# Kernel tuning notes

Measured on AMD Instinct MI355X. Metric: run time of the kernel, lower is better.

The kernel has to match this reference:

```python
import jax, jax.numpy as jnp
import numpy as np

B, NPER, F, D, E, NUM_STEPS = 256, 512, 256, 32, 524288, 4
N = B * NPER
INIT_TAU, TAU_SCALE, STEP_ALPHA = 0.1, 0.5, 5.0


def setup_inputs() -> dict:
    key = jax.random.key(0)
    ks = jax.random.split(key, 10)
    x_start = jax.random.uniform(ks[0], (N,), jnp.float32, 0.1, 1.0)   # strictly positive iterate
    x_solution = jax.random.uniform(ks[1], (N,), jnp.float32, 0.0, 1.0)
    q = jax.random.normal(ks[2], (N,), jnp.float32)
    edge_src = jax.random.randint(ks[3], (E,), 0, N, jnp.int32)
    edge_dst = jax.random.randint(ks[4], (E,), 0, N, jnp.int32)
    vals_batch = jnp.repeat(jnp.arange(B, dtype=jnp.int32), NPER)      # equal-sized graphs
    proj_matrix = jax.random.normal(ks[5], (B, NPER, F), jnp.float32) / np.float32(np.sqrt(NPER))
    W_in = jax.random.normal(ks[6], (2, D), jnp.float32) / np.float32(np.sqrt(2.0))
    b_in = jnp.zeros((D,), jnp.float32)
    W_msg = jax.random.normal(ks[7], (D, D), jnp.float32) / np.float32(np.sqrt(D))
    b_msg = jnp.zeros((D,), jnp.float32)
    W_out = jax.random.normal(ks[8], (D, 1), jnp.float32) / np.float32(np.sqrt(D))
    b_out = jnp.zeros((1,), jnp.float32)
    return {"x_start": x_start, "x_solution": x_solution, "q": q,
            "proj_matrix": proj_matrix, "W_in": W_in, "b_in": b_in,
            "W_msg": W_msg, "b_msg": b_msg, "W_out": W_out, "b_out": b_out,
            "edge_src": edge_src, "edge_dst": edge_dst, "vals_batch": vals_batch}


def _l1_normalize(x, batch):
    # per-graph L1 normalization: x / sum_i |x_i| over the graph segment
    s = jax.ops.segment_sum(jnp.abs(x), batch, num_segments=B)
    return x / (s[batch] + 1e-12)


def _line_search(x, d, batch, max_alpha):
    # largest per-graph alpha s.t. x + alpha*d >= 0, capped at max_alpha
    ratio = jnp.where(d < 0, x / jnp.maximum(-d, 1e-12), max_alpha)
    a = jnp.clip(jax.ops.segment_min(ratio, batch, num_segments=B), 0.0, max_alpha)
    return a[batch]  # gathered back to per-node


def _gnn(xs, q, edge_src, edge_dst, W_in, b_in, W_msg, b_msg, W_out, b_out):
    h = jax.nn.relu(jnp.stack([xs, q], axis=-1) @ W_in + b_in)      # [N, D]
    m = h[edge_src] @ W_msg + b_msg                                  # [E, D]
    agg = jax.ops.segment_sum(m, edge_dst, num_segments=N)          # [N, D]
    h2 = jax.nn.relu(h + agg)
    return h2 @ W_out[:, 0] + b_out[0]                               # [N]


def reference(x_start, x_solution, q, proj_matrix, W_in, b_in, W_msg, b_msg,
              W_out, b_out, edge_src, edge_dst, vals_batch):
    tau = INIT_TAU
    xs = x_start
    preds, labels = [], []
    for _ in range(NUM_STEPS):
        pred = _gnn(xs, q, edge_src, edge_dst, W_in, b_in, W_msg, b_msg, W_out, b_out)
        preds.append(pred)
        labels.append(_l1_normalize(x_solution - xs, vals_batch))
        p = _l1_normalize(jax.lax.stop_gradient(pred), vals_batch)   # .detach() in torch
        direction = p + 3.0 * tau / (xs + tau)
        tau = max(tau * TAU_SCALE, 1e-5)
        # to_dense_batch with equal graph sizes == reshape; project onto nullspace basis
        dd = direction.reshape(B, NPER)
        df = jnp.einsum('bnf,bn->bf', proj_matrix, dd)               # [B, F]
        pproj = jnp.einsum('bnf,bf->bn', proj_matrix, df).reshape(-1)  # [N]
        alpha = _line_search(xs, pproj, vals_batch, STEP_ALPHA) * 0.995
        xs = xs + alpha * pproj
    return jnp.stack(preds, axis=1), jnp.stack(labels, axis=1)       # each [N, NUM_STEPS]
```

## Files before the change

### kernel.cpp

```cpp
#include <hip/hip_runtime.h>

#define BB 256
#define NPER 512
#define FF 256
#define DD 32
#define EE 524288
#define NN (BB*NPER)
#define NSTEPS 4

__device__ __forceinline__ float bflo(unsigned u) { return __uint_as_float(u << 16); }
__device__ __forceinline__ float bfhi(unsigned u) { return __uint_as_float(u & 0xFFFF0000u); }
__device__ __forceinline__ unsigned rtn_bf16(unsigned u) {
    return (u + 0x7FFFu + ((u >> 16) & 1u)) >> 16;
}


__global__ void k_degpack(const int* __restrict__ dst, unsigned* __restrict__ deg,
                          const float* __restrict__ xs0, const float* __restrict__ q,
                          float2* __restrict__ xq) {
    int t = blockIdx.x * blockDim.x + threadIdx.x;
    if (t < NN) { float2 v; v.x = xs0[t]; v.y = q[t]; xq[t] = v; }
    atomicAdd(&deg[dst[t]], 1u);
}

__global__ void k_bsum(const unsigned* __restrict__ deg, unsigned* __restrict__ bsum) {
    __shared__ unsigned r[256];
    int t = threadIdx.x;
    r[t] = deg[blockIdx.x * 256 + t];
    __syncthreads();
    for (int o = 128; o > 0; o >>= 1) { if (t < o) r[t] += r[t + o]; __syncthreads(); }
    if (t == 0) bsum[blockIdx.x] = r[0];
}

__global__ void k_scanb(const unsigned* __restrict__ bsum, unsigned* __restrict__ bbase) {
    __shared__ unsigned r[512];
    int t = threadIdx.x;
    unsigned own = bsum[t];
    r[t] = own;
    __syncthreads();
    for (int o = 1; o < 512; o <<= 1) {
        unsigned v = (t >= o) ? r[t - o] : 0u;
        __syncthreads();
        r[t] += v;
        __syncthreads();
    }
    bbase[t] = r[t] - own;
}

__global__ void k_offsets(const unsigned* __restrict__ deg, const unsigned* __restrict__ bbase,
                          unsigned* __restrict__ rowstart, unsigned* __restrict__ cursor) {
    __shared__ unsigned r[256];
    int t = threadIdx.x;
    int i = blockIdx.x * 256 + t;
    unsigned d = deg[i];
    r[t] = d;
    __syncthreads();
    for (int o = 1; o < 256; o <<= 1) {
        unsigned v = (t >= o) ? r[t - o] : 0u;
        __syncthreads();
        r[t] += v;
        __syncthreads();
    }
    unsigned excl = r[t] - d + bbase[blockIdx.x];
    rowstart[i] = excl;
    cursor[i] = excl;
}

__global__ void k_fill(const int* __restrict__ src, const int* __restrict__ dst,
                       unsigned* __restrict__ cursor, int* __restrict__ csr_src) {
    int e = blockIdx.x * blockDim.x + threadIdx.x;
    unsigned pos = atomicAdd(&cursor[dst[e]], 1u);
    csr_src[pos] = src[e];
}

__global__ __launch_bounds__(256) void k_cast(const float* __restrict__ Pf,
                                              unsigned short* __restrict__ Pbf) {
    size_t idx = ((size_t)blockIdx.x * 256 + threadIdx.x) * 8;
    float4 a = *(const float4*)(Pf + idx);
    float4 c = *(const float4*)(Pf + idx + 4);
    uint4 o;
    o.x = rtn_bf16(__float_as_uint(a.x)) | (rtn_bf16(__float_as_uint(a.y)) << 16);
    o.y = rtn_bf16(__float_as_uint(a.z)) | (rtn_bf16(__float_as_uint(a.w)) << 16);
    o.z = rtn_bf16(__float_as_uint(c.x)) | (rtn_bf16(__float_as_uint(c.y)) << 16);
    o.w = rtn_bf16(__float_as_uint(c.z)) | (rtn_bf16(__float_as_uint(c.w)) << 16);
    *(uint4*)(Pbf + idx) = o;
}


__global__ void k_node_g(const float2* __restrict__ xq,
                         const float* __restrict__ Win, const float* __restrict__ bin,
                         const unsigned* __restrict__ rowstart, const unsigned* __restrict__ deg,
                         const int* __restrict__ csr_src,
                         const float* __restrict__ Wmsg, const float* __restrict__ bmsg,
                         const float* __restrict__ Wout, const float* __restrict__ bout,
                         float* __restrict__ pred, float* __restrict__ out_preds, int step) {
    int tid = threadIdx.x;
    int d = tid & 31;
    int i = blockIdx.x * 8 + (tid >> 5);
    float w0 = Win[d], w1 = Win[DD + d], b0 = bin[d];
    float wcol[DD];
    #pragma unroll
    for (int k = 0; k < DD; ++k) wcol[k] = Wmsg[k * DD + d];
    unsigned rs = rowstart[i];
    unsigned dg = deg[i];
    unsigned nfull = dg < 32u ? dg : 32u;
    float xv = 0.f, qv = 0.f;
    if ((unsigned)d < nfull) {
        int sv = csr_src[rs + d];
        float2 v = xq[sv];
        xv = v.x; qv = v.y;
    }
    float s = 0.f;
    for (unsigned j = 0; j < nfull; ++j) {
        float xj = __shfl(xv, (int)j, 32);
        float qj = __shfl(qv, (int)j, 32);
        s += fmaxf(xj * w0 + qj * w1 + b0, 0.f);
    }
    for (unsigned j = 32; j < dg; ++j) {
        int sv = csr_src[rs + j];
        float2 v = xq[sv];
        s += fmaxf(v.x * w0 + v.y * w1 + b0, 0.f);
    }
    float2 self = xq[i];
    float hval = fmaxf(self.x * w0 + self.y * w1 + b0, 0.f);
    float agg = (float)dg * bmsg[d];
    #pragma unroll
    for (int k = 0; k < DD; ++k) agg += __shfl(s, k, 32) * wcol[k];
    float h2 = fmaxf(hval + agg, 0.f);
    float v = h2 * Wout[d];
    for (int o = 16; o > 0; o >>= 1) v += __shfl_down(v, o, 32);
    if (d == 0) {
        float pr = v + bout[0];
        pred[i] = pr;
        out_preds[i * NSTEPS + step] = pr;
    }
}

__global__ __launch_bounds__(1024) void k_proj(const unsigned short* __restrict__ Pbf,
                                               float2* __restrict__ xq,
                                               const float* __restrict__ xsol,
                                               const float* __restrict__ pred,
                                               float* __restrict__ out_labels,
                                               float tau, int step) {
    __shared__ float dd_l[NPER], x_l[NPER], pp_l[NPER];
    __shared__ float sl[16 * FF];
    __shared__ float dfl[FF];
    __shared__ float redA[16], redB[16], wmin[16];
    int b = blockIdx.x;
    int t = threadIdx.x;
    int w = t >> 6, lane = t & 63;
    int gbase = b * NPER;

    float x = 0.f, r = 0.f, p = 0.f, a1 = 0.f, a2 = 0.f;
    if (t < NPER) {
        x = xq[gbase + t].x;
        r = xsol[gbase + t] - x;
        p = pred[gbase + t];
        a1 = fabsf(r); a2 = fabsf(p);
    }
    #pragma unroll
    for (int o = 32; o > 0; o >>= 1) {
        a1 += __shfl_down(a1, o, 64);
        a2 += __shfl_down(a2, o, 64);
    }
    if (lane == 0) { redA[w] = a1; redB[w] = a2; }
    __syncthreads();
    float Sr = 1e-12f, Sp = 1e-12f;
    #pragma unroll
    for (int k = 0; k < 16; ++k) { Sr += redA[k]; Sp += redB[k]; }
    if (t < NPER) {
        out_labels[(size_t)(gbase + t) * NSTEPS + step] = r / Sr;
        x_l[t] = x;
        dd_l[t] = p / Sp + 3.0f * tau / (x + tau);
    }
    __syncthreads();

    size_t pbase = ((size_t)(gbase + w * 32)) * FF + 4 * lane;
    const uint2* Pr = (const uint2*)(Pbf + pbase);
    unsigned pl[64];
    #pragma unroll
    for (int n = 0; n < 32; ++n) {
        uint2 pv = Pr[(size_t)n * 64];
        pl[2 * n] = pv.x; pl[2 * n + 1] = pv.y;
    }
    float4 acc = {0.f, 0.f, 0.f, 0.f};
    #pragma unroll
    for (int n = 0; n < 32; ++n) {
        float sc = dd_l[w * 32 + n];
        acc.x += bflo(pl[2 * n]) * sc;
        acc.y += bfhi(pl[2 * n]) * sc;
        acc.z += bflo(pl[2 * n + 1]) * sc;
        acc.w += bfhi(pl[2 * n + 1]) * sc;
    }
    ((float4*)sl)[w * 64 + lane] = acc;
    __syncthreads();
    if (t < FF) {
        float v = 0.f;
        #pragma unroll
        for (int k = 0; k < 16; ++k) v += sl[k * FF + t];
        dfl[t] = v;
    }
    __syncthreads();

    float4 dfv = ((const float4*)dfl)[lane];
    float mloc = 5.0f;
    #pragma unroll
    for (int n = 0; n < 32; ++n) {
        float pr = bflo(pl[2 * n]) * dfv.x + bfhi(pl[2 * n]) * dfv.y
                 + bflo(pl[2 * n + 1]) * dfv.z + bfhi(pl[2 * n + 1]) * dfv.w;
        #pragma unroll
        for (int o = 1; o < 64; o <<= 1) pr += __shfl_xor(pr, o, 64);
        if (lane == 0) pp_l[w * 32 + n] = pr;
        float xr = x_l[w * 32 + n];
        float ratio = (pr < 0.f) ? (xr / fmaxf(-pr, 1e-12f)) : 5.0f;
        mloc = fminf(mloc, ratio);
    }
    if (lane == 0) wmin[w] = mloc;
    __syncthreads();

    float mm = wmin[0];
    #pragma unroll
    for (int k = 1; k < 16; ++k) mm = fminf(mm, wmin[k]);
    float alpha = fminf(fmaxf(mm, 0.f), 5.0f) * 0.995f;
    if (t < NPER) xq[gbase + t].x = x_l[t] + alpha * pp_l[t];
}

__global__ __launch_bounds__(512) void k_lab(const float2* __restrict__ xq,
                                             const float* __restrict__ xsol,
                                             float* __restrict__ out_labels, int step) {
    int b = blockIdx.x;
    int t = threadIdx.x;
    int w = t >> 6, lane = t & 63;
    int i = b * NPER + t;
    float x = xq[i].x;
    float r = xsol[i] - x;
    float a1 = fabsf(r);
    #pragma unroll
    for (int o = 32; o > 0; o >>= 1) a1 += __shfl_down(a1, o, 64);
    __shared__ float red[8];
    if (lane == 0) red[w] = a1;
    __syncthreads();
    float Sr = 1e-12f;
    #pragma unroll
    for (int k = 0; k < 8; ++k) Sr += red[k];
    out_labels[(size_t)i * NSTEPS + step] = r / Sr;
}


extern "C" void kernel_launch(void* const* d_in, const int* in_sizes, int n_in,
                              void* d_out, int out_size, void* d_ws, size_t ws_size,
                              hipStream_t stream) {
    const float* x_start = (const float*)d_in[0];
    const float* x_sol   = (const float*)d_in[1];
    const float* q       = (const float*)d_in[2];
    const float* P       = (const float*)d_in[3];
    const float* Win     = (const float*)d_in[4];
    const float* bin     = (const float*)d_in[5];
    const float* Wmsg    = (const float*)d_in[6];
    const float* bmsg    = (const float*)d_in[7];
    const float* Wout    = (const float*)d_in[8];
    const float* bout    = (const float*)d_in[9];
    const int*   esrc    = (const int*)d_in[10];
    const int*   edst    = (const int*)d_in[11];

    float* out_preds  = (float*)d_out;
    float* out_labels = (float*)d_out + (size_t)NN * NSTEPS;

    float* w = (float*)d_ws;
    float2* xq  = (float2*)w; w += 2 * (size_t)NN;
    float* pred  = w; w += NN;
    unsigned* deg      = (unsigned*)w; w += NN;
    unsigned* rowstart = (unsigned*)w; w += NN;
    unsigned* cursor   = (unsigned*)w; w += NN;
    unsigned* bsum     = (unsigned*)w; w += NN / 256;
    unsigned* bbase    = (unsigned*)w; w += NN / 256;
    int* csr_src       = (int*)w;      w += EE;
    unsigned short* Pbf = (unsigned short*)w;

    hipMemsetAsync(deg, 0, NN * sizeof(unsigned), stream);
    k_degpack<<<EE / 256, 256, 0, stream>>>(edst, deg, x_start, q, xq);
    k_cast<<<(NN / 256) * (FF / 8), 256, 0, stream>>>(P, Pbf);
    k_bsum<<<NN / 256, 256, 0, stream>>>(deg, bsum);
    k_scanb<<<1, NN / 256, 0, stream>>>(bsum, bbase);
    k_offsets<<<NN / 256, 256, 0, stream>>>(deg, bbase, rowstart, cursor);
    k_fill<<<EE / 256, 256, 0, stream>>>(esrc, edst, cursor, csr_src);

    float tau = 0.1f;
    for (int step = 0; step < NSTEPS; ++step) {
        k_node_g<<<NN / 8, 256, 0, stream>>>(xq, Win, bin, rowstart, deg, csr_src,
                                             Wmsg, bmsg, Wout, bout, pred, out_preds, step);
        if (step < NSTEPS - 1) {
            k_proj<<<BB, 1024, 0, stream>>>(Pbf, xq, x_sol, pred, out_labels, tau, step);
        } else {
            k_lab<<<BB, 512, 0, stream>>>(xq, x_sol, out_labels, step);
        }
        tau = fmaxf(tau * 0.5f, 1e-5f);
    }
}
```

Before: 544.4 us.

## Split projection into parallel df-accumulate and project-update kernels; fuse prep kernels

The single per-graph projection kernel (256 blocks of 1024 threads) is split in two. k_dfc spreads the first matvec over 8 row-slices per graph (2048 blocks) and combines partial results with atomicAdd into a zeroed df buffer. k_ppu then does the back-projection, line search and update, and on the second-to-last step also writes the final step's labels, which removes the separate label kernel. The degree count, xq packing and bf16 cast of P are merged into one prep kernel, and the df buffer is cleared by the same memset as the degree array. In exchange, the bf16 P matrix is now read twice per step instead of once held in registers, and there is an extra launch per step plus float atomics.

```diff
diff --git a/kernel.cpp b/kernel.cpp
--- a/kernel.cpp
+++ b/kernel.cpp
@@ -15,67 +15,15 @@
 }
 
 
-__global__ void k_degpack(const int* __restrict__ dst, unsigned* __restrict__ deg,
-                          const float* __restrict__ xs0, const float* __restrict__ q,
-                          float2* __restrict__ xq) {
-    int t = blockIdx.x * blockDim.x + threadIdx.x;
-    if (t < NN) { float2 v; v.x = xs0[t]; v.y = q[t]; xq[t] = v; }
-    atomicAdd(&deg[dst[t]], 1u);
-}
-
-__global__ void k_bsum(const unsigned* __restrict__ deg, unsigned* __restrict__ bsum) {
-    __shared__ unsigned r[256];
-    int t = threadIdx.x;
-    r[t] = deg[blockIdx.x * 256 + t];
-    __syncthreads();
-    for (int o = 128; o > 0; o >>= 1) { if (t < o) r[t] += r[t + o]; __syncthreads(); }
-    if (t == 0) bsum[blockIdx.x] = r[0];
-}
-
-__global__ void k_scanb(const unsigned* __restrict__ bsum, unsigned* __restrict__ bbase) {
-    __shared__ unsigned r[512];
-    int t = threadIdx.x;
-    unsigned own = bsum[t];
-    r[t] = own;
-    __syncthreads();
-    for (int o = 1; o < 512; o <<= 1) {
-        unsigned v = (t >= o) ? r[t - o] : 0u;
-        __syncthreads();
-        r[t] += v;
-        __syncthreads();
-    }
-    bbase[t] = r[t] - own;
-}
-
-__global__ void k_offsets(const unsigned* __restrict__ deg, const unsigned* __restrict__ bbase,
-                          unsigned* __restrict__ rowstart, unsigned* __restrict__ cursor) {
-    __shared__ unsigned r[256];
-    int t = threadIdx.x;
-    int i = blockIdx.x * 256 + t;
-    unsigned d = deg[i];
-    r[t] = d;
-    __syncthreads();
-    for (int o = 1; o < 256; o <<= 1) {
-        unsigned v = (t >= o) ? r[t - o] : 0u;
-        __syncthreads();
-        r[t] += v;
-        __syncthreads();
-    }
-    unsigned excl = r[t] - d + bbase[blockIdx.x];
-    rowstart[i] = excl;
-    cursor[i] = excl;
-}
-
-__global__ void k_fill(const int* __restrict__ src, const int* __restrict__ dst,
-                       unsigned* __restrict__ cursor, int* __restrict__ csr_src) {
-    int e = blockIdx.x * blockDim.x + threadIdx.x;
-    unsigned pos = atomicAdd(&cursor[dst[e]], 1u);
-    csr_src[pos] = src[e];
-}
-
-__global__ __launch_bounds__(256) void k_cast(const float* __restrict__ Pf,
-                                              unsigned short* __restrict__ Pbf) {
-    size_t idx = ((size_t)blockIdx.x * 256 + threadIdx.x) * 8;
+__global__ __launch_bounds__(256) void k_prep(const float* __restrict__ Pf,
+                                              unsigned short* __restrict__ Pbf,
+                                              const float* __restrict__ xs0,
+                                              const float* __restrict__ q,
+                                              float2* __restrict__ xq,
+                                              const int* __restrict__ edst,
+                                              unsigned* __restrict__ deg) {
+    size_t g = (size_t)blockIdx.x * 256 + threadIdx.x;
+    size_t idx = g * 8;
     float4 a = *(const float4*)(Pf + idx);
     float4 c = *(const float4*)(Pf + idx + 4);
     uint4 o;
@@ -84,6 +32,58 @@
     o.z = rtn_bf16(__float_as_uint(c.x)) | (rtn_bf16(__float_as_uint(c.y)) << 16);
     o.w = rtn_bf16(__float_as_uint(c.z)) | (rtn_bf16(__float_as_uint(c.w)) << 16);
     *(uint4*)(Pbf + idx) = o;
+    if (g < NN) { float2 v; v.x = xs0[g]; v.y = q[g]; xq[g] = v; }
+    if (g < EE) atomicAdd(&deg[edst[g]], 1u);
+}
+
+__global__ void k_bsum(const unsigned* __restrict__ deg, unsigned* __restrict__ bsum) {
+    __shared__ unsigned r[256];
+    int t = threadIdx.x;
+    r[t] = deg[blockIdx.x * 256 + t];
+    __syncthreads();
+    for (int o = 128; o > 0; o >>= 1) { if (t < o) r[t] += r[t + o]; __syncthreads(); }
+    if (t == 0) bsum[blockIdx.x] = r[0];
+}
+
+__global__ void k_scanb(const unsigned* __restrict__ bsum, unsigned* __restrict__ bbase) {
+    __shared__ unsigned r[512];
+    int t = threadIdx.x;
+    unsigned own = bsum[t];
+    r[t] = own;
+    __syncthreads();
+    for (int o = 1; o < 512; o <<= 1) {
+        unsigned v = (t >= o) ? r[t - o] : 0u;
+        __syncthreads();
+        r[t] += v;
+        __syncthreads();
+    }
+    bbase[t] = r[t] - own;
+}
+
+__global__ void k_offsets(const unsigned* __restrict__ deg, const unsigned* __restrict__ bbase,
+                          unsigned* __restrict__ rowstart, unsigned* __restrict__ cursor) {
+    __shared__ unsigned r[256];
+    int t = threadIdx.x;
+    int i = blockIdx.x * 256 + t;
+    unsigned d = deg[i];
+    r[t] = d;
+    __syncthreads();
+    for (int o = 1; o < 256; o <<= 1) {
+        unsigned v = (t >= o) ? r[t - o] : 0u;
+        __syncthreads();
+        r[t] += v;
+        __syncthreads();
+    }
+    unsigned excl = r[t] - d + bbase[blockIdx.x];
+    rowstart[i] = excl;
+    cursor[i] = excl;
+}
+
+__global__ void k_fill(const int* __restrict__ src, const int* __restrict__ dst,
+                       unsigned* __restrict__ cursor, int* __restrict__ csr_src) {
+    int e = blockIdx.x * blockDim.x + threadIdx.x;
+    unsigned pos = atomicAdd(&cursor[dst[e]], 1u);
+    csr_src[pos] = src[e];
 }
 
 
@@ -136,28 +136,28 @@
     }
 }
 
-__global__ __launch_bounds__(1024) void k_proj(const unsigned short* __restrict__ Pbf,
-                                               float2* __restrict__ xq,
-                                               const float* __restrict__ xsol,
-                                               const float* __restrict__ pred,
-                                               float* __restrict__ out_labels,
-                                               float tau, int step) {
-    __shared__ float dd_l[NPER], x_l[NPER], pp_l[NPER];
-    __shared__ float sl[16 * FF];
-    __shared__ float dfl[FF];
-    __shared__ float redA[16], redB[16], wmin[16];
-    int b = blockIdx.x;
+__global__ __launch_bounds__(256) void k_dfc(const unsigned short* __restrict__ Pbf,
+                                             const float2* __restrict__ xq,
+                                             const float* __restrict__ xsol,
+                                             const float* __restrict__ pred,
+                                             float* __restrict__ out_labels,
+                                             float* __restrict__ df,
+                                             float tau, int step) {
+    __shared__ float dd_l[64];
+    __shared__ float sl[4 * FF];
+    __shared__ float redA[4], redB[4];
+    int blk = blockIdx.x;
+    int b = blk >> 3, s = blk & 7;
     int t = threadIdx.x;
     int w = t >> 6, lane = t & 63;
     int gbase = b * NPER;
 
-    float x = 0.f, r = 0.f, p = 0.f, a1 = 0.f, a2 = 0.f;
-    if (t < NPER) {
-        x = xq[gbase + t].x;
-        r = xsol[gbase + t] - x;
-        p = pred[gbase + t];
-        a1 = fabsf(r); a2 = fabsf(p);
-    }
+    float x0 = xq[gbase + t].x;
+    float x1 = xq[gbase + 256 + t].x;
+    float r0 = xsol[gbase + t] - x0;
+    float r1 = xsol[gbase + 256 + t] - x1;
+    float a1 = fabsf(r0) + fabsf(r1);
+    float a2 = fabsf(pred[gbase + t]) + fabsf(pred[gbase + 256 + t]);
     #pragma unroll
     for (int o = 32; o > 0; o >>= 1) {
         a1 += __shfl_down(a1, o, 64);
@@ -165,85 +165,91 @@
     }
     if (lane == 0) { redA[w] = a1; redB[w] = a2; }
     __syncthreads();
-    float Sr = 1e-12f, Sp = 1e-12f;
-    #pragma unroll
-    for (int k = 0; k < 16; ++k) { Sr += redA[k]; Sp += redB[k]; }
-    if (t < NPER) {
-        out_labels[(size_t)(gbase + t) * NSTEPS + step] = r / Sr;
-        x_l[t] = x;
-        dd_l[t] = p / Sp + 3.0f * tau / (x + tau);
-    }
-    __syncthreads();
-
-    size_t pbase = ((size_t)(gbase + w * 32)) * FF + 4 * lane;
+    float Sr = 1e-12f + redA[0] + redA[1] + redA[2] + redA[3];
+    float Sp = 1e-12f + redB[0] + redB[1] + redB[2] + redB[3];
+    if (s == 0) {
+        out_labels[(size_t)(gbase + t) * NSTEPS + step] = r0 / Sr;
+        out_labels[(size_t)(gbase + 256 + t) * NSTEPS + step] = r1 / Sr;
+    }
+    if (t < 64) {
+        int row = s * 64 + t;
+        float xx = xq[gbase + row].x;
+        dd_l[t] = pred[gbase + row] / Sp + 3.0f * tau / (xx + tau);
+    }
+    __syncthreads();
+
+    size_t pbase = ((size_t)(gbase + s * 64 + w * 16)) * FF + 4 * lane;
     const uint2* Pr = (const uint2*)(Pbf + pbase);
-    unsigned pl[64];
+    float4 acc = {0.f, 0.f, 0.f, 0.f};
+    #pragma unroll
+    for (int n = 0; n < 16; ++n) {
+        uint2 pv = Pr[(size_t)n * 64];
+        float sc = dd_l[w * 16 + n];
+        acc.x += bflo(pv.x) * sc; acc.y += bfhi(pv.x) * sc;
+        acc.z += bflo(pv.y) * sc; acc.w += bfhi(pv.y) * sc;
+    }
+    ((float4*)sl)[w * 64 + lane] = acc;
+    __syncthreads();
+    if (t < FF) {
+        float v = sl[t] + sl[FF + t] + sl[2 * FF + t] + sl[3 * FF + t];
+        atomicAdd(&df[(size_t)(step * BB + b) * FF + t], v);
+    }
+}
+
+__global__ __launch_bounds__(1024) void k_ppu(const unsigned short* __restrict__ Pbf,
+                                              const float* __restrict__ df,
+                                              float2* __restrict__ xq,
+                                              const float* __restrict__ xsol,
+                                              float* __restrict__ out_labels,
+                                              int step, int last) {
+    __shared__ float x_l[NPER], pp_l[NPER], dfl[FF];
+    __shared__ float wmin[16], red[16];
+    int b = blockIdx.x;
+    int t = threadIdx.x;
+    int w = t >> 6, lane = t & 63;
+    int gbase = b * NPER;
+    if (t < FF) dfl[t] = df[(size_t)(step * BB + b) * FF + t];
+    if (t < NPER) x_l[t] = xq[gbase + t].x;
+    __syncthreads();
+
+    float4 dfv = ((const float4*)dfl)[lane];
+    const uint2* Pr = (const uint2*)(Pbf + ((size_t)(gbase + w * 32)) * FF + 4 * lane);
+    float mloc = 5.0f;
     #pragma unroll
     for (int n = 0; n < 32; ++n) {
         uint2 pv = Pr[(size_t)n * 64];
-        pl[2 * n] = pv.x; pl[2 * n + 1] = pv.y;
-    }
-    float4 acc = {0.f, 0.f, 0.f, 0.f};
-    #pragma unroll
-    for (int n = 0; n < 32; ++n) {
-        float sc = dd_l[w * 32 + n];
-        acc.x += bflo(pl[2 * n]) * sc;
-        acc.y += bfhi(pl[2 * n]) * sc;
-        acc.z += bflo(pl[2 * n + 1]) * sc;
-        acc.w += bfhi(pl[2 * n + 1]) * sc;
-    }
-    ((float4*)sl)[w * 64 + lane] = acc;
-    __syncthreads();
-    if (t < FF) {
-        float v = 0.f;
-        #pragma unroll
-        for (int k = 0; k < 16; ++k) v += sl[k * FF + t];
-        dfl[t] = v;
-    }
-    __syncthreads();
-
-    float4 dfv = ((const float4*)dfl)[lane];
-    float mloc = 5.0f;
-    #pragma unroll
-    for (int n = 0; n < 32; ++n) {
-        float pr = bflo(pl[2 * n]) * dfv.x + bfhi(pl[2 * n]) * dfv.y
-                 + bflo(pl[2 * n + 1]) * dfv.z + bfhi(pl[2 * n + 1]) * dfv.w;
+        float pr = bflo(pv.x) * dfv.x + bfhi(pv.x) * dfv.y
+                 + bflo(pv.y) * dfv.z + bfhi(pv.y) * dfv.w;
         #pragma unroll
         for (int o = 1; o < 64; o <<= 1) pr += __shfl_xor(pr, o, 64);
-        if (lane == 0) pp_l[w * 32 + n] = pr;
-        float xr = x_l[w * 32 + n];
-        float ratio = (pr < 0.f) ? (xr / fmaxf(-pr, 1e-12f)) : 5.0f;
+        int row = w * 32 + n;
+        if (lane == 0) pp_l[row] = pr;
+        float ratio = (pr < 0.f) ? (x_l[row] / fmaxf(-pr, 1e-12f)) : 5.0f;
         mloc = fminf(mloc, ratio);
     }
     if (lane == 0) wmin[w] = mloc;
     __syncthreads();
-
     float mm = wmin[0];
     #pragma unroll
     for (int k = 1; k < 16; ++k) mm = fminf(mm, wmin[k]);
     float alpha = fminf(fmaxf(mm, 0.f), 5.0f) * 0.995f;
-    if (t < NPER) xq[gbase + t].x = x_l[t] + alpha * pp_l[t];
-}
-
-__global__ __launch_bounds__(512) void k_lab(const float2* __restrict__ xq,
-                                             const float* __restrict__ xsol,
-                                             float* __restrict__ out_labels, int step) {
-    int b = blockIdx.x;
-    int t = threadIdx.x;
-    int w = t >> 6, lane = t & 63;
-    int i = b * NPER + t;
-    float x = xq[i].x;
-    float r = xsol[i] - x;
-    float a1 = fabsf(r);
-    #pragma unroll
-    for (int o = 32; o > 0; o >>= 1) a1 += __shfl_down(a1, o, 64);
-    __shared__ float red[8];
-    if (lane == 0) red[w] = a1;
-    __syncthreads();
-    float Sr = 1e-12f;
-    #pragma unroll
-    for (int k = 0; k < 8; ++k) Sr += red[k];
-    out_labels[(size_t)i * NSTEPS + step] = r / Sr;
+    float xnew = 0.f;
+    if (t < NPER) {
+        xnew = x_l[t] + alpha * pp_l[t];
+        xq[gbase + t].x = xnew;
+    }
+    if (last) {
+        float r = 0.f, a1 = 0.f;
+        if (t < NPER) { r = xsol[gbase + t] - xnew; a1 = fabsf(r); }
+        #pragma unroll
+        for (int o = 32; o > 0; o >>= 1) a1 += __shfl_down(a1, o, 64);
+        if (lane == 0) red[w] = a1;
+        __syncthreads();
+        float Sr = 1e-12f;
+        #pragma unroll
+        for (int k = 0; k < 16; ++k) Sr += red[k];
+        if (t < NPER) out_labels[(size_t)(gbase + t) * NSTEPS + (NSTEPS - 1)] = r / Sr;
+    }
 }
 
 
@@ -267,9 +273,10 @@
     float* out_labels = (float*)d_out + (size_t)NN * NSTEPS;
 
     float* w = (float*)d_ws;
+    unsigned* deg = (unsigned*)w;      w += NN;
+    float* df     = w;                 w += (size_t)3 * BB * FF;
     float2* xq  = (float2*)w; w += 2 * (size_t)NN;
     float* pred  = w; w += NN;
-    unsigned* deg      = (unsigned*)w; w += NN;
     unsigned* rowstart = (unsigned*)w; w += NN;
     unsigned* cursor   = (unsigned*)w; w += NN;
     unsigned* bsum     = (unsigned*)w; w += NN / 256;
@@ -277,9 +284,8 @@
     int* csr_src       = (int*)w;      w += EE;
     unsigned short* Pbf = (unsigned short*)w;
 
-    hipMemsetAsync(deg, 0, NN * sizeof(unsigned), stream);
-    k_degpack<<<EE / 256, 256, 0, stream>>>(edst, deg, x_start, q, xq);
-    k_cast<<<(NN / 256) * (FF / 8), 256, 0, stream>>>(P, Pbf);
+    hipMemsetAsync(deg, 0, (NN + (size_t)3 * BB * FF) * sizeof(unsigned), stream);
+    k_prep<<<(NN / 256) * (FF / 8), 256, 0, stream>>>(P, Pbf, x_start, q, xq, edst, deg);
     k_bsum<<<NN / 256, 256, 0, stream>>>(deg, bsum);
     k_scanb<<<1, NN / 256, 0, stream>>>(bsum, bbase);
     k_offsets<<<NN / 256, 256, 0, stream>>>(deg, bbase, rowstart, cursor);
@@ -290,9 +296,9 @@
         k_node_g<<<NN / 8, 256, 0, stream>>>(xq, Win, bin, rowstart, deg, csr_src,
                                              Wmsg, bmsg, Wout, bout, pred, out_preds, step);
         if (step < NSTEPS - 1) {
-            k_proj<<<BB, 1024, 0, stream>>>(Pbf, xq, x_sol, pred, out_labels, tau, step);
-        } else {
-            k_lab<<<BB, 512, 0, stream>>>(xq, x_sol, out_labels, step);
+            k_dfc<<<BB * 8, 256, 0, stream>>>(Pbf, xq, x_sol, pred, out_labels, df, tau, step);
+            k_ppu<<<BB, 1024, 0, stream>>>(Pbf, df, xq, x_sol, out_labels,
+                                           step, step == NSTEPS - 2 ? 1 : 0);
         }
         tau = fmaxf(tau * 0.5f, 1e-5f);
     }
```

New measurement: 525.4 us. -3.5%, faster.
